# Kernel optimization log

Hardware: AMD Instinct MI355X
Metric: run time of the kernel (lower is better)

The kernel has to match this reference:

```python
import jax, jax.numpy as jnp
import numpy as np

N_NODES = 100_000
EMB = 64
M1 = 500_000   # unary relation ground atoms
M2 = 1_000_000 # binary relation ground atoms


def _mlp_params(key, d_in, d_hid, d_out):
    k1, k2 = jax.random.split(key)
    W1 = jax.random.normal(k1, (d_in, d_hid), jnp.float32) / np.sqrt(d_in)
    W2 = jax.random.normal(k2, (d_hid, d_out), jnp.float32) / np.sqrt(d_hid)
    return W1, jnp.zeros((d_hid,), jnp.float32), W2, jnp.zeros((d_out,), jnp.float32)


def setup_inputs() -> dict:
    key = jax.random.key(0)
    kx, k1, k2, km1, km2, ku = jax.random.split(key, 6)
    node_embeddings = jax.random.normal(kx, (N_NODES, EMB), jnp.float32)
    rel1_idx = jax.random.randint(k1, (M1, 1), 0, N_NODES, jnp.int64)
    rel2_idx = jax.random.randint(k2, (M2, 2), 0, N_NODES, jnp.int64)
    msg1_W1, msg1_b1, msg1_W2, msg1_b2 = _mlp_params(km1, EMB, EMB, EMB)
    msg2_W1, msg2_b1, msg2_W2, msg2_b2 = _mlp_params(km2, 2 * EMB, 2 * EMB, 2 * EMB)
    upd_W1, upd_b1, upd_W2, upd_b2 = _mlp_params(ku, 2 * EMB, EMB, EMB)
    return dict(node_embeddings=node_embeddings, rel1_idx=rel1_idx, rel2_idx=rel2_idx,
                msg1_W1=msg1_W1, msg1_b1=msg1_b1, msg1_W2=msg1_W2, msg1_b2=msg1_b2,
                msg2_W1=msg2_W1, msg2_b1=msg2_b1, msg2_W2=msg2_W2, msg2_b2=msg2_b2,
                upd_W1=upd_W1, upd_b1=upd_b1, upd_W2=upd_W2, upd_b2=upd_b2)


def _relation_messages(node_emb, idx, W1, b1, W2, b2):
    """Gather arity argument embeddings, run MLP, return per-argument messages
    flattened to [M*arity, EMB] plus flat scatter indices [M*arity]."""
    M, arity = idx.shape
    g = node_emb[idx].reshape(M, arity * EMB)          # gather + concat args
    h = jax.nn.relu(g @ W1 + b1)
    m = (h @ W2 + b2).reshape(M * arity, EMB)          # one message per arg slot
    return m, idx.reshape(-1)


def reference(node_embeddings, rel1_idx, rel2_idx,
              msg1_W1, msg1_b1, msg1_W2, msg1_b2,
              msg2_W1, msg2_b1, msg2_W2, msg2_b2,
              upd_W1, upd_b1, upd_W2, upd_b2):
    n = node_embeddings.shape[0]
    # message computation per relation
    m1, i1 = _relation_messages(node_embeddings, rel1_idx, msg1_W1, msg1_b1, msg1_W2, msg1_b2)
    m2, i2 = _relation_messages(node_embeddings, rel2_idx, msg2_W1, msg2_b1, msg2_W2, msg2_b2)
    # scatter-sum aggregation into node slots
    agg = jax.ops.segment_sum(m1, i1, num_segments=n)
    agg = agg + jax.ops.segment_sum(m2, i2, num_segments=n)
    # node update MLP on [node, aggregated]
    u = jnp.concatenate([node_embeddings, agg], axis=-1)   # [N, 2E]
    return jax.nn.relu(u @ upd_W1 + upd_b1) @ upd_W2 + upd_b2
```

## Files before the change

### kernel.cpp

```cpp
#include <hip/hip_runtime.h>
#include <hip/hip_fp16.h>

typedef __bf16 bf16;
typedef bf16 bf16x8 __attribute__((ext_vector_type(8)));
typedef float f32x4 __attribute__((ext_vector_type(4)));

#define LD64  80
#define LD128 144

static __device__ __forceinline__ f32x4 mfma16(bf16x8 a, bf16x8 b, f32x4 c) {
    return __builtin_amdgcn_mfma_f32_16x16x32_bf16(a, b, c, 0, 0, 0);
}

static __device__ __forceinline__ bf16x8 cvt8(float4 a, float4 b) {
    bf16x8 v;
    v[0] = (bf16)a.x; v[1] = (bf16)a.y; v[2] = (bf16)a.z; v[3] = (bf16)a.w;
    v[4] = (bf16)b.x; v[5] = (bf16)b.y; v[6] = (bf16)b.z; v[7] = (bf16)b.w;
    return v;
}

static __device__ __forceinline__ uint32_t pack_bf16(float lo, float hi) {
    bf16 a = (bf16)lo, b = (bf16)hi;
    uint16_t ua = *(uint16_t*)&a, ub = *(uint16_t*)&b;
    return ((uint32_t)ub << 16) | (uint32_t)ua;
}

static __device__ __forceinline__ uint32_t pack_f16(float lo, float hi) {
    __half hl = __float2half_rn(lo), hh = __float2half_rn(hi);
    uint16_t a = *(uint16_t*)&hl, b = *(uint16_t*)&hh;
    return ((uint32_t)b << 16) | (uint32_t)a;
}
static __device__ __forceinline__ void atomic_pk_f16(__half* addr, uint32_t v) {
    asm volatile("global_atomic_pk_add_f16 %0, %1, off" :: "v"(addr), "v"(v) : "memory");
}
static __device__ __forceinline__ float h2f_lo(uint32_t u) {
    uint16_t s = (uint16_t)u; __half h = *(__half*)&s; return __half2float(h);
}
static __device__ __forceinline__ float h2f_hi(uint32_t u) {
    uint16_t s = (uint16_t)(u >> 16); __half h = *(__half*)&s; return __half2float(h);
}

__global__ __launch_bounds__(256) void hist_rk_kernel(
    const int* __restrict__ r1, const int* __restrict__ r2,
    unsigned* __restrict__ cnt1, unsigned* __restrict__ cnt2,
    unsigned short* __restrict__ rk, int M1, int M2x2)
{
    int i = blockIdx.x * 256 + threadIdx.x;
    const int T = gridDim.x * 256;
    const int tot = M1 + M2x2;
    for (; i < tot; i += T) {
        if (i < M1) {
            atomicAdd(&cnt1[r1[i]], 1u);
        } else {
            const int j = i - M1;
            unsigned r = atomicAdd(&cnt2[r2[j]], 1u);
            rk[j] = (unsigned short)r;
        }
    }
}

__global__ __launch_bounds__(256) void scan_sums(
    const unsigned* __restrict__ cnt, unsigned* __restrict__ csum)
{
    __shared__ unsigned s[256];
    const int b = blockIdx.x, t = threadIdx.x;
    s[t] = cnt[b * 512 + t] + cnt[b * 512 + 256 + t];
    __syncthreads();
    for (int d = 128; d > 0; d >>= 1) {
        if (t < d) s[t] += s[t + d];
        __syncthreads();
    }
    if (t == 0) csum[b] = s[0];
}

__global__ __launch_bounds__(256) void scan_chunkoff(unsigned* __restrict__ csum, int nch) {
    __shared__ unsigned s[2][256];
    const int t = threadIdx.x;
    if (nch > 256) {
        if (t == 0) {
            unsigned run = 0;
            for (int j = 0; j < nch; ++j) { unsigned v = csum[j]; csum[j] = run; run += v; }
        }
        return;
    }
    unsigned v = (t < nch) ? csum[t] : 0u;
    s[0][t] = v;
    __syncthreads();
    int src = 0;
    for (int d = 1; d < 256; d <<= 1) {
        int dst = src ^ 1;
        s[dst][t] = s[src][t] + (t >= d ? s[src][t - d] : 0u);
        __syncthreads();
        src = dst;
    }
    if (t < nch) csum[t] = s[src][t] - v;
}

__global__ __launch_bounds__(256) void scan_apply(
    const unsigned* __restrict__ cnt, const unsigned* __restrict__ csum,
    unsigned* __restrict__ rowp)
{
    __shared__ unsigned s[2][512];
    const int b = blockIdx.x, t = threadIdx.x;
    const unsigned base = csum[b];
    s[0][t] = cnt[b * 512 + t];
    s[0][t + 256] = cnt[b * 512 + t + 256];
    __syncthreads();
    int src = 0;
    for (int d = 1; d < 512; d <<= 1) {
        int dst = src ^ 1;
        for (int i = t; i < 512; i += 256)
            s[dst][i] = s[src][i] + (i >= d ? s[src][i - d] : 0u);
        __syncthreads();
        src = dst;
    }
    for (int i = t; i < 512; i += 256)
        rowp[b * 512 + i] = base + s[src][i] - cnt[b * 512 + i];
}

__global__ __launch_bounds__(256) void mix_kernel(
    const int* __restrict__ r2, const unsigned short* __restrict__ rk,
    const unsigned* __restrict__ rowp, int2* __restrict__ sp2,
    int M2x2, int SB,
    const float* __restrict__ emb,
    const float* __restrict__ mW1, const float* __restrict__ mb1,
    const float* __restrict__ r1W1, const float* __restrict__ r1b1,
    const float* __restrict__ r1W2, const float* __restrict__ r1b2,
    bf16* __restrict__ P0, bf16* __restrict__ P1,
    float* __restrict__ aggu, int N, int PT)
{
    __shared__ bf16 sG[64 * LD64];
    __shared__ bf16 sH[64 * LD64];
    __shared__ bf16 sW1t[64 * LD64];
    __shared__ bf16 sW2t[64 * LD64];
    __shared__ float sB1[64], sB2[64];

    const int t = threadIdx.x;

    if ((int)blockIdx.x < SB) {
        const int T = SB * 256;
        for (int i = blockIdx.x * 256 + t; i < M2x2; i += T) {
            const int2 pr = *(const int2*)(r2 + (i & ~1));
            const int slot = i & 1;
            const int n = slot ? pr.y : pr.x;
            const unsigned pos = rowp[n] + (unsigned)rk[i];
            sp2[pos] = make_int2((pr.x << 1) | slot, pr.y);
        }
        return;
    }

    const int bid = blockIdx.x - SB;
    const int G = gridDim.x - SB;
    const int wave = t >> 6, lane = t & 63;
    const int l15 = lane & 15, quad = lane >> 4;
    const int r = t >> 2, p = t & 3;

    for (int i = t; i < 64 * 64; i += 256) {
        int k = i >> 6, n = i & 63;
        sW1t[n * LD64 + k] = (bf16)r1W1[i];
        sW2t[n * LD64 + k] = (bf16)r1W2[i];
    }
    if (t < 64) { sB1[t] = r1b1[t]; sB2[t] = r1b2[t]; }

    bf16x8 wf0[2][2], wf1[2][2];
    float biasv[2];
    #pragma unroll
    for (int j = 0; j < 2; ++j) {
        const int n = (wave * 2 + j) * 16 + l15;
        biasv[j] = mb1[n];
        #pragma unroll
        for (int kt = 0; kt < 2; ++kt) {
            bf16x8 f0, f1;
            #pragma unroll
            for (int e = 0; e < 8; ++e) {
                int k = kt * 32 + quad * 8 + e;
                f0[e] = (bf16)mW1[k * 128 + n];
                f1[e] = (bf16)mW1[(64 + k) * 128 + n];
            }
            wf0[j][kt] = f0;
            wf1[j][kt] = f1;
        }
    }

    for (int tile = bid; tile < PT; tile += G) {
        __syncthreads();
        const int base = tile * 64;
        const int R = base + r;
        if (R < N) {
            const float4* src = (const float4*)(emb + (size_t)R * 64 + p * 16);
            float4 v0 = src[0], v1 = src[1], v2 = src[2], v3 = src[3];
            *(bf16x8*)&sG[r * LD64 + p * 16 + 0] = cvt8(v0, v1);
            *(bf16x8*)&sG[r * LD64 + p * 16 + 8] = cvt8(v2, v3);
        }
        __syncthreads();

        f32x4 a0[4][2], a1[4][2];
        #pragma unroll
        for (int mt = 0; mt < 4; ++mt)
            #pragma unroll
            for (int j = 0; j < 2; ++j) {
                a0[mt][j] = (f32x4){0.f, 0.f, 0.f, 0.f};
                a1[mt][j] = (f32x4){0.f, 0.f, 0.f, 0.f};
            }
        #pragma unroll
        for (int mt = 0; mt < 4; ++mt)
            #pragma unroll
            for (int kt = 0; kt < 2; ++kt) {
                bf16x8 a = *(const bf16x8*)&sG[(mt * 16 + l15) * LD64 + kt * 32 + quad * 8];
                #pragma unroll
                for (int j = 0; j < 2; ++j) {
                    a0[mt][j] = mfma16(a, wf0[j][kt], a0[mt][j]);
                    a1[mt][j] = mfma16(a, wf1[j][kt], a1[mt][j]);
                }
            }
        #pragma unroll
        for (int mt = 0; mt < 4; ++mt)
            #pragma unroll
            for (int j = 0; j < 2; ++j) {
                const int colb = (wave * 2 + j) * 16 + (l15 & ~1);
                const int odd = l15 & 1;
                #pragma unroll
                for (int rr = 0; rr < 4; ++rr) {
                    float v = a0[mt][j][rr] + biasv[j];
                    float o = __shfl_xor(v, 1);
                    float w = a1[mt][j][rr];
                    float ow = __shfl_xor(w, 1);
                    if ((rr >> 1) == odd) {
                        int node = base + mt * 16 + quad * 4 + rr;
                        if (node < N) {
                            *(uint32_t*)&P0[(size_t)node * 128 + colb] =
                                odd ? pack_bf16(o, v) : pack_bf16(v, o);
                            *(uint32_t*)&P1[(size_t)node * 128 + colb] =
                                odd ? pack_bf16(ow, w) : pack_bf16(w, ow);
                        }
                    }
                }
            }

        f32x4 acc[4];
        #pragma unroll
        for (int nt = 0; nt < 4; ++nt) acc[nt] = (f32x4){0.f, 0.f, 0.f, 0.f};
        #pragma unroll
        for (int kt = 0; kt < 2; ++kt) {
            bf16x8 a = *(const bf16x8*)&sG[(wave * 16 + l15) * LD64 + kt * 32 + quad * 8];
            #pragma unroll
            for (int nt = 0; nt < 4; ++nt) {
                bf16x8 bfr = *(const bf16x8*)&sW1t[(nt * 16 + l15) * LD64 + kt * 32 + quad * 8];
                acc[nt] = mfma16(a, bfr, acc[nt]);
            }
        }
        #pragma unroll
        for (int nt = 0; nt < 4; ++nt) {
            float bias = sB1[nt * 16 + l15];
            #pragma unroll
            for (int rr = 0; rr < 4; ++rr) {
                float v = acc[nt][rr] + bias;
                v = v > 0.f ? v : 0.f;
                sH[(wave * 16 + quad * 4 + rr) * LD64 + nt * 16 + l15] = (bf16)v;
            }
        }
        __syncthreads();

        f32x4 acc2[4];
        #pragma unroll
        for (int nt = 0; nt < 4; ++nt) acc2[nt] = (f32x4){0.f, 0.f, 0.f, 0.f};
        #pragma unroll
        for (int kt = 0; kt < 2; ++kt) {
            bf16x8 a = *(const bf16x8*)&sH[(wave * 16 + l15) * LD64 + kt * 32 + quad * 8];
            #pragma unroll
            for (int nt = 0; nt < 4; ++nt) {
                bf16x8 bfr = *(const bf16x8*)&sW2t[(nt * 16 + l15) * LD64 + kt * 32 + quad * 8];
                acc2[nt] = mfma16(a, bfr, acc2[nt]);
            }
        }
        #pragma unroll
        for (int nt = 0; nt < 4; ++nt) {
            float bias = sB2[nt * 16 + l15];
            #pragma unroll
            for (int rr = 0; rr < 4; ++rr) {
                int row = wave * 16 + quad * 4 + rr;
                int R2 = base + row;
                if (R2 < N)
                    aggu[(size_t)R2 * 64 + nt * 16 + l15] = acc2[nt][rr] + bias;
            }
        }
    }
}

__global__ __launch_bounds__(256) void rel2_fused_kernel(
    const bf16* __restrict__ P0, const bf16* __restrict__ P1,
    const int2* __restrict__ sp2,
    const unsigned* __restrict__ rowp, const unsigned* __restrict__ cnt1,
    const float* __restrict__ W2, const float* __restrict__ b2,
    float* agg, int N, int numGroups)
{
    const int HLD = 136;
    __shared__ bf16 hT[2][32 * 136];
    __shared__ float sCf[2][32];

    const int t = threadIdx.x;
    const int wave = t >> 6, lane = t & 63;
    const int l15 = lane & 15, quad = lane >> 4;

    bf16x8 w2f[2][4];
    #pragma unroll
    for (int s = 0; s < 2; ++s)
        #pragma unroll
        for (int kt = 0; kt < 4; ++kt) {
            bf16x8 f;
            #pragma unroll
            for (int e = 0; e < 8; ++e) {
                int k = kt * 32 + quad * 8 + e;
                f[e] = (bf16)W2[k * 128 + s * 64 + wave * 16 + l15];
            }
            w2f[s][kt] = f;
        }
    const int col = wave * 16 + l15;
    const float b2a = b2[col], b2b = b2[64 + col];

    for (int g = blockIdx.x; g < numGroups; g += gridDim.x) {
        const int gb = g * 32;
        __syncthreads();

        for (int k = 0; k < 8; ++k) {
            const int n = gb + wave * 8 + k;
            float a0lo = 0.f, a0hi = 0.f, a1lo = 0.f, a1hi = 0.f;
            float c0 = 0.f, c1 = 0.f;
            if (n < N) {
                unsigned e = rowp[n];
                const unsigned end = rowp[n + 1];
                while (e < end) {
                    const int cnt = (int)min(64u, end - e);
                    int pk = 0, pi1 = 0;
                    if ((int)lane < cnt) {
                        const int2 v = sp2[e + lane];
                        pk = v.x; pi1 = v.y;
                    }
                    unsigned long long bm =
                        __ballot(((int)lane < cnt) && (pk & 1));
                    const int n1 = __popcll(bm);
                    c1 += (float)n1;
                    c0 += (float)(cnt - n1);

                    int j = 0;
                    for (; j + 8 <= cnt; j += 8) {
                        uint32_t d0v[8], d1v[8]; int ajv[8];
                        #pragma unroll
                        for (int q = 0; q < 8; ++q) {
                            const int aj = __shfl(pk, j + q);
                            const int u1 = __shfl(pi1, j + q);
                            ajv[q] = aj;
                            d0v[q] = *(const uint32_t*)(P0 + (size_t)(aj >> 1) * 128 + lane * 2);
                            d1v[q] = *(const uint32_t*)(P1 + (size_t)u1 * 128 + lane * 2);
                        }
                        #pragma unroll
                        for (int q = 0; q < 8; ++q) {
                            float lo = __uint_as_float(d0v[q] << 16) + __uint_as_float(d1v[q] << 16);
                            float hi = __uint_as_float(d0v[q] & 0xffff0000u) + __uint_as_float(d1v[q] & 0xffff0000u);
                            lo = fmaxf(lo, 0.f); hi = fmaxf(hi, 0.f);
                            if (ajv[q] & 1) { a1lo += lo; a1hi += hi; }
                            else            { a0lo += lo; a0hi += hi; }
                        }
                    }
                    for (; j + 4 <= cnt; j += 4) {
                        uint32_t d0v[4], d1v[4]; int ajv[4];
                        #pragma unroll
                        for (int q = 0; q < 4; ++q) {
                            const int aj = __shfl(pk, j + q);
                            const int u1 = __shfl(pi1, j + q);
                            ajv[q] = aj;
                            d0v[q] = *(const uint32_t*)(P0 + (size_t)(aj >> 1) * 128 + lane * 2);
                            d1v[q] = *(const uint32_t*)(P1 + (size_t)u1 * 128 + lane * 2);
                        }
                        #pragma unroll
                        for (int q = 0; q < 4; ++q) {
                            float lo = __uint_as_float(d0v[q] << 16) + __uint_as_float(d1v[q] << 16);
                            float hi = __uint_as_float(d0v[q] & 0xffff0000u) + __uint_as_float(d1v[q] & 0xffff0000u);
                            lo = fmaxf(lo, 0.f); hi = fmaxf(hi, 0.f);
                            if (ajv[q] & 1) { a1lo += lo; a1hi += hi; }
                            else            { a0lo += lo; a0hi += hi; }
                        }
                    }
                    for (; j < cnt; ++j) {
                        const int aj = __shfl(pk, j);
                        const int u1 = __shfl(pi1, j);
                        const uint32_t d0 = *(const uint32_t*)(P0 + (size_t)(aj >> 1) * 128 + lane * 2);
                        const uint32_t d1 = *(const uint32_t*)(P1 + (size_t)u1 * 128 + lane * 2);
                        float lo = __uint_as_float(d0 << 16) + __uint_as_float(d1 << 16);
                        float hi = __uint_as_float(d0 & 0xffff0000u) + __uint_as_float(d1 & 0xffff0000u);
                        lo = fmaxf(lo, 0.f); hi = fmaxf(hi, 0.f);
                        if (aj & 1) { a1lo += lo; a1hi += hi; }
                        else        { a0lo += lo; a0hi += hi; }
                    }
                    e += cnt;
                }
            }
            const int row = wave * 8 + k;
            *(uint32_t*)&hT[0][row * HLD + lane * 2] = pack_bf16(a0lo, a0hi);
            *(uint32_t*)&hT[1][row * HLD + lane * 2] = pack_bf16(a1lo, a1hi);
            if (lane == 0) { sCf[0][row] = c0; sCf[1][row] = c1; }
        }
        __syncthreads();

        f32x4 acc[2];
        #pragma unroll
        for (int mt = 0; mt < 2; ++mt) acc[mt] = (f32x4){0.f, 0.f, 0.f, 0.f};
        #pragma unroll
        for (int s = 0; s < 2; ++s)
            #pragma unroll
            for (int mt = 0; mt < 2; ++mt)
                #pragma unroll
                for (int kt = 0; kt < 4; ++kt) {
                    bf16x8 a = *(const bf16x8*)&hT[s][(mt * 16 + l15) * HLD + kt * 32 + quad * 8];
                    acc[mt] = mfma16(a, w2f[s][kt], acc[mt]);
                }
        #pragma unroll
        for (int mt = 0; mt < 2; ++mt)
            #pragma unroll
            for (int rr = 0; rr < 4; ++rr) {
                const int row = mt * 16 + quad * 4 + rr;
                const int n = gb + row;
                if (n < N) {
                    float* ap = agg + (size_t)n * 64 + col;
                    const float au = *ap;
                    *ap = (float)cnt1[n] * au + acc[mt][rr]
                        + sCf[0][row] * b2a + sCf[1][row] * b2b;
                }
            }
    }
}

__global__ __launch_bounds__(256) void update_kernel(
    const float* __restrict__ emb, const float* agg,
    const float* __restrict__ W1, const float* __restrict__ b1,
    const float* __restrict__ W2, const float* __restrict__ b2,
    float* out, int N, int numTiles)
{
    __shared__ bf16 sW1t[64 * LD128];
    __shared__ bf16 sW2t[64 * LD64];
    __shared__ bf16 sU[64 * LD128];
    __shared__ bf16 sH[64 * LD64];
    __shared__ float sB1[64], sB2[64];

    const int t = threadIdx.x;
    const int wave = t >> 6, lane = t & 63;
    const int l15 = lane & 15, quad = lane >> 4;
    const int r = t >> 2, p = t & 3;

    for (int i = t; i < 128 * 64; i += 256) {
        int k = i >> 6, n = i & 63;
        sW1t[n * LD128 + k] = (bf16)W1[i];
    }
    for (int i = t; i < 64 * 64; i += 256) {
        int k = i >> 6, n = i & 63;
        sW2t[n * LD64 + k] = (bf16)W2[i];
    }
    if (t < 64) { sB1[t] = b1[t]; sB2[t] = b2[t]; }

    for (int tile = blockIdx.x; tile < numTiles; tile += gridDim.x) {
        __syncthreads();
        const int base = tile * 64;
        {
            const int R = base + r;
            if (R < N) {
                const float* srcp = (p < 2) ? (emb + (size_t)R * 64 + p * 32)
                                            : (agg + (size_t)R * 64 + (p - 2) * 32);
                const float4* src = (const float4*)srcp;
                #pragma unroll
                for (int i = 0; i < 4; ++i)
                    *(bf16x8*)&sU[r * LD128 + p * 32 + i * 8] = cvt8(src[2 * i], src[2 * i + 1]);
            }
        }
        __syncthreads();

        f32x4 acc[4];
        #pragma unroll
        for (int nt = 0; nt < 4; ++nt) acc[nt] = (f32x4){0.f, 0.f, 0.f, 0.f};
        #pragma unroll
        for (int kt = 0; kt < 4; ++kt) {
            bf16x8 a = *(const bf16x8*)&sU[(wave * 16 + l15) * LD128 + kt * 32 + quad * 8];
            #pragma unroll
            for (int nt = 0; nt < 4; ++nt) {
                bf16x8 bfr = *(const bf16x8*)&sW1t[(nt * 16 + l15) * LD128 + kt * 32 + quad * 8];
                acc[nt] = mfma16(a, bfr, acc[nt]);
            }
        }
        #pragma unroll
        for (int nt = 0; nt < 4; ++nt) {
            float bias = sB1[nt * 16 + l15];
            #pragma unroll
            for (int rr = 0; rr < 4; ++rr) {
                float v = acc[nt][rr] + bias;
                v = v > 0.f ? v : 0.f;
                sH[(wave * 16 + quad * 4 + rr) * LD64 + nt * 16 + l15] = (bf16)v;
            }
        }
        __syncthreads();

        f32x4 acc2[4];
        #pragma unroll
        for (int nt = 0; nt < 4; ++nt) acc2[nt] = (f32x4){0.f, 0.f, 0.f, 0.f};
        #pragma unroll
        for (int kt = 0; kt < 2; ++kt) {
            bf16x8 a = *(const bf16x8*)&sH[(wave * 16 + l15) * LD64 + kt * 32 + quad * 8];
            #pragma unroll
            for (int nt = 0; nt < 4; ++nt) {
                bf16x8 bfr = *(const bf16x8*)&sW2t[(nt * 16 + l15) * LD64 + kt * 32 + quad * 8];
                acc2[nt] = mfma16(a, bfr, acc2[nt]);
            }
        }
        #pragma unroll
        for (int nt = 0; nt < 4; ++nt) {
            float bias = sB2[nt * 16 + l15];
            #pragma unroll
            for (int rr = 0; rr < 4; ++rr) {
                int row = wave * 16 + quad * 4 + rr;
                int R = base + row;
                if (R < N)
                    out[(size_t)R * 64 + nt * 16 + l15] = acc2[nt][rr] + bias;
            }
        }
    }
}

__global__ __launch_bounds__(256) void rel1_fb_kernel(
    const float* __restrict__ emb, const int* __restrict__ idx,
    const float* __restrict__ W1, const float* __restrict__ b1,
    const float* __restrict__ W2, const float* __restrict__ b2,
    __half* __restrict__ agg, int M, int numTiles)
{
    __shared__ bf16 sW1t[64 * LD64];
    __shared__ bf16 sW2t[64 * LD64];
    __shared__ bf16 sG[64 * LD64];
    __shared__ bf16 sH[64 * LD64];
    __shared__ float sB1[64], sB2[64];
    __shared__ int sIdx[64];

    const int t = threadIdx.x;
    const int wave = t >> 6, lane = t & 63;
    const int l15 = lane & 15, quad = lane >> 4;
    const int r = t >> 2, p = t & 3;

    for (int i = t; i < 64 * 64; i += 256) {
        int k = i >> 6, n = i & 63;
        sW1t[n * LD64 + k] = (bf16)W1[i];
        sW2t[n * LD64 + k] = (bf16)W2[i];
    }
    if (t < 64) { sB1[t] = b1[t]; sB2[t] = b2[t]; }

    for (int tile = blockIdx.x; tile < numTiles; tile += gridDim.x) {
        __syncthreads();
        const int base = tile * 64;
        int id = -1;
        { int R = base + r; if (R < M) id = idx[R]; }
        if (p == 0) sIdx[r] = id;
        if (id >= 0) {
            const float4* src = (const float4*)(emb + (size_t)id * 64 + p * 16);
            float4 v0 = src[0], v1 = src[1], v2 = src[2], v3 = src[3];
            *(bf16x8*)&sG[r * LD64 + p * 16 + 0] = cvt8(v0, v1);
            *(bf16x8*)&sG[r * LD64 + p * 16 + 8] = cvt8(v2, v3);
        }
        __syncthreads();

        f32x4 acc[4];
        #pragma unroll
        for (int nt = 0; nt < 4; ++nt) acc[nt] = (f32x4){0.f, 0.f, 0.f, 0.f};
        #pragma unroll
        for (int kt = 0; kt < 2; ++kt) {
            bf16x8 a = *(const bf16x8*)&sG[(wave * 16 + l15) * LD64 + kt * 32 + quad * 8];
            #pragma unroll
            for (int nt = 0; nt < 4; ++nt) {
                bf16x8 bfr = *(const bf16x8*)&sW1t[(nt * 16 + l15) * LD64 + kt * 32 + quad * 8];
                acc[nt] = mfma16(a, bfr, acc[nt]);
            }
        }
        #pragma unroll
        for (int nt = 0; nt < 4; ++nt) {
            float bias = sB1[nt * 16 + l15];
            #pragma unroll
            for (int rr = 0; rr < 4; ++rr) {
                float v = acc[nt][rr] + bias;
                v = v > 0.f ? v : 0.f;
                sH[(wave * 16 + quad * 4 + rr) * LD64 + nt * 16 + l15] = (bf16)v;
            }
        }
        __syncthreads();

        f32x4 acc2[4];
        #pragma unroll
        for (int nt = 0; nt < 4; ++nt) acc2[nt] = (f32x4){0.f, 0.f, 0.f, 0.f};
        #pragma unroll
        for (int kt = 0; kt < 2; ++kt) {
            bf16x8 a = *(const bf16x8*)&sH[(wave * 16 + l15) * LD64 + kt * 32 + quad * 8];
            #pragma unroll
            for (int nt = 0; nt < 4; ++nt) {
                bf16x8 bfr = *(const bf16x8*)&sW2t[(nt * 16 + l15) * LD64 + kt * 32 + quad * 8];
                acc2[nt] = mfma16(a, bfr, acc2[nt]);
            }
        }
        #pragma unroll
        for (int nt = 0; nt < 4; ++nt) {
            float bias = sB2[nt * 16 + l15];
            const int colb = nt * 16 + (l15 & ~1);
            const int odd = l15 & 1;
            #pragma unroll
            for (int rr = 0; rr < 4; ++rr) {
                float v = acc2[nt][rr] + bias;
                float o = __shfl_xor(v, 1);
                if ((rr >> 1) == odd) {
                    int row = wave * 16 + quad * 4 + rr;
                    int id2 = sIdx[row];
                    if (id2 >= 0)
                        atomic_pk_f16(agg + (size_t)id2 * 64 + colb,
                                      odd ? pack_f16(o, v) : pack_f16(v, o));
                }
            }
        }
    }
}

__global__ __launch_bounds__(256) void rel2_fb_kernel(
    const float* __restrict__ emb, const int* __restrict__ idx,
    const float* __restrict__ W1, const float* __restrict__ b1,
    const float* __restrict__ W2, const float* __restrict__ b2,
    __half* __restrict__ agg, int M, int numTiles)
{
    __shared__ bf16 sG[64 * LD128];
    __shared__ bf16 sH[64 * LD128];
    __shared__ int sIdx[128];

    const int t = threadIdx.x;
    const int wave = t >> 6, lane = t & 63;
    const int l15 = lane & 15, quad = lane >> 4;
    const int r = t >> 2, p = t & 3;

    bf16x8 w1f[2][4], w2f[2][4];
    float bias1[2], bias2[2];
    #pragma unroll
    for (int j = 0; j < 2; ++j) {
        const int n = (wave * 2 + j) * 16 + l15;
        bias1[j] = b1[n];
        bias2[j] = b2[n];
        #pragma unroll
        for (int kt = 0; kt < 4; ++kt) {
            bf16x8 f1, f2;
            #pragma unroll
            for (int e = 0; e < 8; ++e) {
                int k = kt * 32 + quad * 8 + e;
                f1[e] = (bf16)W1[k * 128 + n];
                f2[e] = (bf16)W2[k * 128 + n];
            }
            w1f[j][kt] = f1;
            w2f[j][kt] = f2;
        }
    }

    for (int tile = blockIdx.x; tile < numTiles; tile += gridDim.x) {
        __syncthreads();
        const int base = tile * 64;
        int i0 = -1, i1 = -1;
        { int R = base + r; if (R < M) { i0 = idx[R * 2]; i1 = idx[R * 2 + 1]; } }
        if (p == 0) { sIdx[r * 2] = i0; sIdx[r * 2 + 1] = i1; }
        {
            int myid = (p < 2) ? i0 : i1;
            if (myid >= 0) {
                const float4* src = (const float4*)(emb + (size_t)myid * 64 + (p & 1) * 32);
                #pragma unroll
                for (int i = 0; i < 4; ++i)
                    *(bf16x8*)&sG[r * LD128 + p * 32 + i * 8] = cvt8(src[2 * i], src[2 * i + 1]);
            }
        }
        __syncthreads();

        f32x4 acc[4][2];
        #pragma unroll
        for (int mt = 0; mt < 4; ++mt)
            #pragma unroll
            for (int j = 0; j < 2; ++j) acc[mt][j] = (f32x4){0.f, 0.f, 0.f, 0.f};
        #pragma unroll
        for (int mt = 0; mt < 4; ++mt) {
            #pragma unroll
            for (int kt = 0; kt < 4; ++kt) {
                bf16x8 a = *(const bf16x8*)&sG[(mt * 16 + l15) * LD128 + kt * 32 + quad * 8];
                #pragma unroll
                for (int j = 0; j < 2; ++j) acc[mt][j] = mfma16(a, w1f[j][kt], acc[mt][j]);
            }
        }
        #pragma unroll
        for (int mt = 0; mt < 4; ++mt)
            #pragma unroll
            for (int j = 0; j < 2; ++j) {
                #pragma unroll
                for (int rr = 0; rr < 4; ++rr) {
                    float v = acc[mt][j][rr] + bias1[j];
                    v = v > 0.f ? v : 0.f;
                    sH[(mt * 16 + quad * 4 + rr) * LD128 + (wave * 2 + j) * 16 + l15] = (bf16)v;
                }
            }
        __syncthreads();

        f32x4 acc2[4][2];
        #pragma unroll
        for (int mt = 0; mt < 4; ++mt)
            #pragma unroll
            for (int j = 0; j < 2; ++j) acc2[mt][j] = (f32x4){0.f, 0.f, 0.f, 0.f};
        #pragma unroll
        for (int mt = 0; mt < 4; ++mt) {
            #pragma unroll
            for (int kt = 0; kt < 4; ++kt) {
                bf16x8 a = *(const bf16x8*)&sH[(mt * 16 + l15) * LD128 + kt * 32 + quad * 8];
                #pragma unroll
                for (int j = 0; j < 2; ++j) acc2[mt][j] = mfma16(a, w2f[j][kt], acc2[mt][j]);
            }
        }
        #pragma unroll
        for (int mt = 0; mt < 4; ++mt) {
            #pragma unroll
            for (int j = 0; j < 2; ++j) {
                const int colb = (wave * 2 + j) * 16 + (l15 & ~1);
                const int sel = colb >> 6;
                const int c = colb & 63;
                const int odd = l15 & 1;
                #pragma unroll
                for (int rr = 0; rr < 4; ++rr) {
                    float v = acc2[mt][j][rr] + bias2[j];
                    float o = __shfl_xor(v, 1);
                    if ((rr >> 1) == odd) {
                        int row = mt * 16 + quad * 4 + rr;
                        int id2 = sIdx[row * 2 + sel];
                        if (id2 >= 0)
                            atomic_pk_f16(agg + (size_t)id2 * 64 + c,
                                          odd ? pack_f16(o, v) : pack_f16(v, o));
                    }
                }
            }
        }
    }
}

__global__ __launch_bounds__(256) void update_fb_kernel(
    const float* __restrict__ emb, const __half* __restrict__ agg,
    const float* __restrict__ W1, const float* __restrict__ b1,
    const float* __restrict__ W2, const float* __restrict__ b2,
    float* __restrict__ out, int N, int numTiles)
{
    __shared__ bf16 sW1t[64 * LD128];
    __shared__ bf16 sW2t[64 * LD64];
    __shared__ bf16 sU[64 * LD128];
    __shared__ bf16 sH[64 * LD64];
    __shared__ float sB1[64], sB2[64];

    const int t = threadIdx.x;
    const int wave = t >> 6, lane = t & 63;
    const int l15 = lane & 15, quad = lane >> 4;
    const int r = t >> 2, p = t & 3;

    for (int i = t; i < 128 * 64; i += 256) {
        int k = i >> 6, n = i & 63;
        sW1t[n * LD128 + k] = (bf16)W1[i];
    }
    for (int i = t; i < 64 * 64; i += 256) {
        int k = i >> 6, n = i & 63;
        sW2t[n * LD64 + k] = (bf16)W2[i];
    }
    if (t < 64) { sB1[t] = b1[t]; sB2[t] = b2[t]; }

    for (int tile = blockIdx.x; tile < numTiles; tile += gridDim.x) {
        __syncthreads();
        const int base = tile * 64;
        {
            const int R = base + r;
            if (R < N) {
                if (p < 2) {
                    const float4* src = (const float4*)(emb + (size_t)R * 64 + p * 32);
                    #pragma unroll
                    for (int i = 0; i < 4; ++i)
                        *(bf16x8*)&sU[r * LD128 + p * 32 + i * 8] = cvt8(src[2 * i], src[2 * i + 1]);
                } else {
                    const uint4* src = (const uint4*)(agg + (size_t)R * 64 + (p - 2) * 32);
                    #pragma unroll
                    for (int i = 0; i < 4; ++i) {
                        uint4 u = src[i];
                        bf16x8 o;
                        o[0] = (bf16)h2f_lo(u.x); o[1] = (bf16)h2f_hi(u.x);
                        o[2] = (bf16)h2f_lo(u.y); o[3] = (bf16)h2f_hi(u.y);
                        o[4] = (bf16)h2f_lo(u.z); o[5] = (bf16)h2f_hi(u.z);
                        o[6] = (bf16)h2f_lo(u.w); o[7] = (bf16)h2f_hi(u.w);
                        *(bf16x8*)&sU[r * LD128 + p * 32 + i * 8] = o;
                    }
                }
            }
        }
        __syncthreads();

        f32x4 acc[4];
        #pragma unroll
        for (int nt = 0; nt < 4; ++nt) acc[nt] = (f32x4){0.f, 0.f, 0.f, 0.f};
        #pragma unroll
        for (int kt = 0; kt < 4; ++kt) {
            bf16x8 a = *(const bf16x8*)&sU[(wave * 16 + l15) * LD128 + kt * 32 + quad * 8];
            #pragma unroll
            for (int nt = 0; nt < 4; ++nt) {
                bf16x8 bfr = *(const bf16x8*)&sW1t[(nt * 16 + l15) * LD128 + kt * 32 + quad * 8];
                acc[nt] = mfma16(a, bfr, acc[nt]);
            }
        }
        #pragma unroll
        for (int nt = 0; nt < 4; ++nt) {
            float bias = sB1[nt * 16 + l15];
            #pragma unroll
            for (int rr = 0; rr < 4; ++rr) {
                float v = acc[nt][rr] + bias;
                v = v > 0.f ? v : 0.f;
                sH[(wave * 16 + quad * 4 + rr) * LD64 + nt * 16 + l15] = (bf16)v;
            }
        }
        __syncthreads();

        f32x4 acc2[4];
        #pragma unroll
        for (int nt = 0; nt < 4; ++nt) acc2[nt] = (f32x4){0.f, 0.f, 0.f, 0.f};
        #pragma unroll
        for (int kt = 0; kt < 2; ++kt) {
            bf16x8 a = *(const bf16x8*)&sH[(wave * 16 + l15) * LD64 + kt * 32 + quad * 8];
            #pragma unroll
            for (int nt = 0; nt < 4; ++nt) {
                bf16x8 bfr = *(const bf16x8*)&sW2t[(nt * 16 + l15) * LD64 + kt * 32 + quad * 8];
                acc2[nt] = mfma16(a, bfr, acc2[nt]);
            }
        }
        #pragma unroll
        for (int nt = 0; nt < 4; ++nt) {
            float bias = sB2[nt * 16 + l15];
            #pragma unroll
            for (int rr = 0; rr < 4; ++rr) {
                int row = wave * 16 + quad * 4 + rr;
                int R = base + row;
                if (R < N)
                    out[(size_t)R * 64 + nt * 16 + l15] = acc2[nt][rr] + bias;
            }
        }
    }
}

extern "C" void kernel_launch(void* const* d_in, const int* in_sizes, int n_in,
                              void* d_out, int out_size, void* d_ws, size_t ws_size,
                              hipStream_t stream) {
    const float* emb    = (const float*)d_in[0];
    const int*   rel1   = (const int*)d_in[1];
    const int*   rel2   = (const int*)d_in[2];
    const float* m1W1   = (const float*)d_in[3];
    const float* m1b1   = (const float*)d_in[4];
    const float* m1W2   = (const float*)d_in[5];
    const float* m1b2   = (const float*)d_in[6];
    const float* m2W1   = (const float*)d_in[7];
    const float* m2b1   = (const float*)d_in[8];
    const float* m2W2   = (const float*)d_in[9];
    const float* m2b2   = (const float*)d_in[10];
    const float* uW1    = (const float*)d_in[11];
    const float* ub1    = (const float*)d_in[12];
    const float* uW2    = (const float*)d_in[13];
    const float* ub2    = (const float*)d_in[14];

    const int N    = in_sizes[0] / 64;
    const int M1   = in_sizes[1];
    const int M2x2 = in_sizes[2];
    const int M2   = M2x2 / 2;

    const int nch   = (N + 511) / 512;
    const int nbins = nch * 512;
    const int nbuckets = (N + 31) / 32;
    char* wsb = (char*)d_ws;
    size_t off = 0;
    auto take = [&](size_t bytes) {
        size_t cur = off;
        off = (off + bytes + 255) & ~(size_t)255;
        return cur;
    };
    bf16*           P0   = (bf16*)          (wsb + take((size_t)N * 128 * sizeof(bf16)));
    bf16*           P1   = (bf16*)          (wsb + take((size_t)N * 128 * sizeof(bf16)));
    unsigned*       cnt1 = (unsigned*)      (wsb + take((size_t)nbins * 4));
    unsigned*       cnt2 = (unsigned*)      (wsb + take((size_t)nbins * 4));
    unsigned*       rowp = (unsigned*)      (wsb + take((size_t)nbins * 4));
    unsigned*       csum = (unsigned*)      (wsb + take((size_t)(nch + 64) * 4));
    unsigned short* rk   = (unsigned short*)(wsb + take((size_t)M2x2 * 2));
    int2*           sp2  = (int2*)          (wsb + take((size_t)M2x2 * 8));

    if (off <= ws_size) {
        float* agg = (float*)d_out;

        hipMemsetAsync(cnt1, 0, (size_t)((char*)rowp - (char*)cnt1), stream);

        const int gh = 2048;
        hist_rk_kernel<<<gh, 256, 0, stream>>>(rel1, rel2, cnt1, cnt2, rk, M1, M2x2);

        scan_sums<<<nch, 256, 0, stream>>>(cnt2, csum);
        scan_chunkoff<<<1, 256, 0, stream>>>(csum, nch);
        scan_apply<<<nch, 256, 0, stream>>>(cnt2, csum, rowp);

        const int SB = 2048;
        const int PT = (N + 63) / 64;
        mix_kernel<<<SB + PT, 256, 0, stream>>>(
            rel2, rk, rowp, sp2, M2x2, SB,
            emb, m2W1, m2b1, m1W1, m1b1, m1W2, m1b2,
            P0, P1, agg, N, PT);

        const int gf = nbuckets < 2048 ? nbuckets : 2048;
        rel2_fused_kernel<<<gf, 256, 0, stream>>>(
            P0, P1, sp2, rowp, cnt1, m2W2, m2b2, agg, N, nbuckets);

        update_kernel<<<PT, 256, 0, stream>>>(emb, agg, uW1, ub1, uW2, ub2,
                                              (float*)d_out, N, PT);
    } else {
        __half* aggh = (__half*)d_ws;
        hipMemsetAsync(aggh, 0, (size_t)N * 64 * sizeof(__half), stream);

        const int t1 = (M1 + 63) / 64;
        rel1_fb_kernel<<<t1 < 1024 ? t1 : 1024, 256, 0, stream>>>(
            emb, rel1, m1W1, m1b1, m1W2, m1b2, aggh, M1, t1);
        const int t2 = (M2 + 63) / 64;
        rel2_fb_kernel<<<t2 < 2048 ? t2 : 2048, 256, 0, stream>>>(
            emb, rel2, m2W1, m2b1, m2W2, m2b2, aggh, M2, t2);
        const int tu = (N + 63) / 64;
        update_fb_kernel<<<tu, 256, 0, stream>>>(emb, aggh, uW1, ub1, uW2, ub2,
                                                 (float*)d_out, N, tu);
    }
}
```

Measured before the change: 431.7 us.

## Split per-node edge lists by slot and gather only partner rows

Builds separate histograms for slot-0 and slot-1 occurrences, so each node's CSR segment is partitioned by slot, and stores only the partner index (4 bytes) instead of an int2 per entry. The fused rel2 kernel loads the node's own P0/P1 row once per segment and gathers only the partner's projection per edge. This halves gather traffic per edge and removes the per-edge slot branch and ballot. The cost is an extra counter array and extra reads in the scan kernels.

```diff
diff --git a/kernel.cpp b/kernel.cpp
--- a/kernel.cpp
+++ b/kernel.cpp
@@ -42,29 +42,33 @@
 
 __global__ __launch_bounds__(256) void hist_rk_kernel(
     const int* __restrict__ r1, const int* __restrict__ r2,
-    unsigned* __restrict__ cnt1, unsigned* __restrict__ cnt2,
-    unsigned short* __restrict__ rk, int M1, int M2x2)
+    unsigned* __restrict__ cnt1, unsigned* __restrict__ cntA,
+    unsigned* __restrict__ cntB, ushort2* __restrict__ rk2, int M1, int M2)
 {
     int i = blockIdx.x * 256 + threadIdx.x;
     const int T = gridDim.x * 256;
-    const int tot = M1 + M2x2;
+    const int tot = M1 + M2;
     for (; i < tot; i += T) {
         if (i < M1) {
             atomicAdd(&cnt1[r1[i]], 1u);
         } else {
-            const int j = i - M1;
-            unsigned r = atomicAdd(&cnt2[r2[j]], 1u);
-            rk[j] = (unsigned short)r;
+            const int e = i - M1;
+            const int2 pr = *(const int2*)(r2 + 2 * e);
+            unsigned ra = atomicAdd(&cntA[pr.x], 1u);
+            unsigned rb = atomicAdd(&cntB[pr.y], 1u);
+            rk2[e] = make_ushort2((unsigned short)ra, (unsigned short)rb);
         }
     }
 }
 
 __global__ __launch_bounds__(256) void scan_sums(
-    const unsigned* __restrict__ cnt, unsigned* __restrict__ csum)
+    const unsigned* __restrict__ cntA, const unsigned* __restrict__ cntB,
+    unsigned* __restrict__ csum)
 {
     __shared__ unsigned s[256];
     const int b = blockIdx.x, t = threadIdx.x;
-    s[t] = cnt[b * 512 + t] + cnt[b * 512 + 256 + t];
+    const int x = b * 512 + t, y = x + 256;
+    s[t] = cntA[x] + cntB[x] + cntA[y] + cntB[y];
     __syncthreads();
     for (int d = 128; d > 0; d >>= 1) {
         if (t < d) s[t] += s[t + d];
@@ -97,14 +101,14 @@
 }
 
 __global__ __launch_bounds__(256) void scan_apply(
-    const unsigned* __restrict__ cnt, const unsigned* __restrict__ csum,
-    unsigned* __restrict__ rowp)
+    const unsigned* __restrict__ cntA, const unsigned* __restrict__ cntB,
+    const unsigned* __restrict__ csum, unsigned* __restrict__ rowp)
 {
     __shared__ unsigned s[2][512];
     const int b = blockIdx.x, t = threadIdx.x;
     const unsigned base = csum[b];
-    s[0][t] = cnt[b * 512 + t];
-    s[0][t + 256] = cnt[b * 512 + t + 256];
+    s[0][t] = cntA[b * 512 + t] + cntB[b * 512 + t];
+    s[0][t + 256] = cntA[b * 512 + t + 256] + cntB[b * 512 + t + 256];
     __syncthreads();
     int src = 0;
     for (int d = 1; d < 512; d <<= 1) {
@@ -114,14 +118,16 @@
         __syncthreads();
         src = dst;
     }
-    for (int i = t; i < 512; i += 256)
-        rowp[b * 512 + i] = base + s[src][i] - cnt[b * 512 + i];
+    for (int i = t; i < 512; i += 256) {
+        const unsigned tot = cntA[b * 512 + i] + cntB[b * 512 + i];
+        rowp[b * 512 + i] = base + s[src][i] - tot;
+    }
 }
 
 __global__ __launch_bounds__(256) void mix_kernel(
-    const int* __restrict__ r2, const unsigned short* __restrict__ rk,
-    const unsigned* __restrict__ rowp, int2* __restrict__ sp2,
-    int M2x2, int SB,
+    const int* __restrict__ r2, const ushort2* __restrict__ rk2,
+    const unsigned* __restrict__ rowp, const unsigned* __restrict__ cntA,
+    int* __restrict__ sps, int M2, int SB,
     const float* __restrict__ emb,
     const float* __restrict__ mW1, const float* __restrict__ mb1,
     const float* __restrict__ r1W1, const float* __restrict__ r1b1,
@@ -139,12 +145,11 @@
 
     if ((int)blockIdx.x < SB) {
         const int T = SB * 256;
-        for (int i = blockIdx.x * 256 + t; i < M2x2; i += T) {
-            const int2 pr = *(const int2*)(r2 + (i & ~1));
-            const int slot = i & 1;
-            const int n = slot ? pr.y : pr.x;
-            const unsigned pos = rowp[n] + (unsigned)rk[i];
-            sp2[pos] = make_int2((pr.x << 1) | slot, pr.y);
+        for (int e = blockIdx.x * 256 + t; e < M2; e += T) {
+            const int2 pr = *(const int2*)(r2 + 2 * e);
+            const ushort2 rr = rk2[e];
+            sps[rowp[pr.x] + (unsigned)rr.x] = pr.y;
+            sps[rowp[pr.y] + cntA[pr.y] + (unsigned)rr.y] = pr.x;
         }
         return;
     }
@@ -287,10 +292,63 @@
     }
 }
 
+static __device__ __forceinline__ void seg_walk(
+    const int* __restrict__ sps, unsigned s, const unsigned e,
+    const bf16* __restrict__ P, const int lane,
+    const float clo, const float chi, float& alo, float& ahi)
+{
+    while (s < e) {
+        const int cnt = (int)min(64u, e - s);
+        int pid = 0;
+        if (lane < cnt) pid = sps[s + lane];
+        int j = 0;
+        for (; j + 8 <= cnt; j += 8) {
+            uint32_t dv[8];
+            #pragma unroll
+            for (int q = 0; q < 8; ++q) {
+                const int id = __shfl(pid, j + q);
+                dv[q] = *(const uint32_t*)(P + (size_t)id * 128 + lane * 2);
+            }
+            #pragma unroll
+            for (int q = 0; q < 8; ++q) {
+                float lo = __uint_as_float(dv[q] << 16) + clo;
+                float hi = __uint_as_float(dv[q] & 0xffff0000u) + chi;
+                alo += fmaxf(lo, 0.f);
+                ahi += fmaxf(hi, 0.f);
+            }
+        }
+        for (; j + 4 <= cnt; j += 4) {
+            uint32_t dv[4];
+            #pragma unroll
+            for (int q = 0; q < 4; ++q) {
+                const int id = __shfl(pid, j + q);
+                dv[q] = *(const uint32_t*)(P + (size_t)id * 128 + lane * 2);
+            }
+            #pragma unroll
+            for (int q = 0; q < 4; ++q) {
+                float lo = __uint_as_float(dv[q] << 16) + clo;
+                float hi = __uint_as_float(dv[q] & 0xffff0000u) + chi;
+                alo += fmaxf(lo, 0.f);
+                ahi += fmaxf(hi, 0.f);
+            }
+        }
+        for (; j < cnt; ++j) {
+            const int id = __shfl(pid, j);
+            const uint32_t d = *(const uint32_t*)(P + (size_t)id * 128 + lane * 2);
+            float lo = __uint_as_float(d << 16) + clo;
+            float hi = __uint_as_float(d & 0xffff0000u) + chi;
+            alo += fmaxf(lo, 0.f);
+            ahi += fmaxf(hi, 0.f);
+        }
+        s += cnt;
+    }
+}
+
 __global__ __launch_bounds__(256) void rel2_fused_kernel(
     const bf16* __restrict__ P0, const bf16* __restrict__ P1,
-    const int2* __restrict__ sp2,
-    const unsigned* __restrict__ rowp, const unsigned* __restrict__ cnt1,
+    const int* __restrict__ sps,
+    const unsigned* __restrict__ rowp, const unsigned* __restrict__ cntA,
+    const unsigned* __restrict__ cnt1,
     const float* __restrict__ W2, const float* __restrict__ b2,
     float* agg, int N, int numGroups)
 {
@@ -324,81 +382,30 @@
 
         for (int k = 0; k < 8; ++k) {
             const int n = gb + wave * 8 + k;
-            float a0lo = 0.f, a0hi = 0.f, a1lo = 0.f, a1hi = 0.f;
-            float c0 = 0.f, c1 = 0.f;
+            float h0lo = 0.f, h0hi = 0.f, h1lo = 0.f, h1hi = 0.f;
+            float c0f = 0.f, c1f = 0.f;
             if (n < N) {
-                unsigned e = rowp[n];
-                const unsigned end = rowp[n + 1];
-                while (e < end) {
-                    const int cnt = (int)min(64u, end - e);
-                    int pk = 0, pi1 = 0;
-                    if ((int)lane < cnt) {
-                        const int2 v = sp2[e + lane];
-                        pk = v.x; pi1 = v.y;
-                    }
-                    unsigned long long bm =
-                        __ballot(((int)lane < cnt) && (pk & 1));
-                    const int n1 = __popcll(bm);
-                    c1 += (float)n1;
-                    c0 += (float)(cnt - n1);
-
-                    int j = 0;
-                    for (; j + 8 <= cnt; j += 8) {
-                        uint32_t d0v[8], d1v[8]; int ajv[8];
-                        #pragma unroll
-                        for (int q = 0; q < 8; ++q) {
-                            const int aj = __shfl(pk, j + q);
-                            const int u1 = __shfl(pi1, j + q);
-                            ajv[q] = aj;
-                            d0v[q] = *(const uint32_t*)(P0 + (size_t)(aj >> 1) * 128 + lane * 2);
-                            d1v[q] = *(const uint32_t*)(P1 + (size_t)u1 * 128 + lane * 2);
-                        }
-                        #pragma unroll
-                        for (int q = 0; q < 8; ++q) {
-                            float lo = __uint_as_float(d0v[q] << 16) + __uint_as_float(d1v[q] << 16);
-                            float hi = __uint_as_float(d0v[q] & 0xffff0000u) + __uint_as_float(d1v[q] & 0xffff0000u);
-                            lo = fmaxf(lo, 0.f); hi = fmaxf(hi, 0.f);
-                            if (ajv[q] & 1) { a1lo += lo; a1hi += hi; }
-                            else            { a0lo += lo; a0hi += hi; }
-                        }
-                    }
-                    for (; j + 4 <= cnt; j += 4) {
-                        uint32_t d0v[4], d1v[4]; int ajv[4];
-                        #pragma unroll
-                        for (int q = 0; q < 4; ++q) {
-                            const int aj = __shfl(pk, j + q);
-                            const int u1 = __shfl(pi1, j + q);
-                            ajv[q] = aj;
-                            d0v[q] = *(const uint32_t*)(P0 + (size_t)(aj >> 1) * 128 + lane * 2);
-                            d1v[q] = *(const uint32_t*)(P1 + (size_t)u1 * 128 + lane * 2);
-                        }
-                        #pragma unroll
-                        for (int q = 0; q < 4; ++q) {
-                            float lo = __uint_as_float(d0v[q] << 16) + __uint_as_float(d1v[q] << 16);
-                            float hi = __uint_as_float(d0v[q] & 0xffff0000u) + __uint_as_float(d1v[q] & 0xffff0000u);
-                            lo = fmaxf(lo, 0.f); hi = fmaxf(hi, 0.f);
-                            if (ajv[q] & 1) { a1lo += lo; a1hi += hi; }
-                            else            { a0lo += lo; a0hi += hi; }
-                        }
-                    }
-                    for (; j < cnt; ++j) {
-                        const int aj = __shfl(pk, j);
-                        const int u1 = __shfl(pi1, j);
-                        const uint32_t d0 = *(const uint32_t*)(P0 + (size_t)(aj >> 1) * 128 + lane * 2);
-                        const uint32_t d1 = *(const uint32_t*)(P1 + (size_t)u1 * 128 + lane * 2);
-                        float lo = __uint_as_float(d0 << 16) + __uint_as_float(d1 << 16);
-                        float hi = __uint_as_float(d0 & 0xffff0000u) + __uint_as_float(d1 & 0xffff0000u);
-                        lo = fmaxf(lo, 0.f); hi = fmaxf(hi, 0.f);
-                        if (aj & 1) { a1lo += lo; a1hi += hi; }
-                        else        { a0lo += lo; a0hi += hi; }
-                    }
-                    e += cnt;
+                const unsigned e0 = rowp[n], e1 = rowp[n + 1];
+                const unsigned cA = cntA[n];
+                c0f = (float)cA;
+                c1f = (float)(e1 - e0 - cA);
+                if (cA) {
+                    const uint32_t pd = *(const uint32_t*)(P0 + (size_t)n * 128 + lane * 2);
+                    const float clo = __uint_as_float(pd << 16);
+                    const float chi = __uint_as_float(pd & 0xffff0000u);
+                    seg_walk(sps, e0, e0 + cA, P1, lane, clo, chi, h0lo, h0hi);
                 }
+                if (e1 > e0 + cA) {
+                    const uint32_t pd = *(const uint32_t*)(P1 + (size_t)n * 128 + lane * 2);
+                    const float clo = __uint_as_float(pd << 16);
+                    const float chi = __uint_as_float(pd & 0xffff0000u);
+                    seg_walk(sps, e0 + cA, e1, P0, lane, clo, chi, h1lo, h1hi);
+                }
             }
             const int row = wave * 8 + k;
-            *(uint32_t*)&hT[0][row * HLD + lane * 2] = pack_bf16(a0lo, a0hi);
-            *(uint32_t*)&hT[1][row * HLD + lane * 2] = pack_bf16(a1lo, a1hi);
-            if (lane == 0) { sCf[0][row] = c0; sCf[1][row] = c1; }
+            *(uint32_t*)&hT[0][row * HLD + lane * 2] = pack_bf16(h0lo, h0hi);
+            *(uint32_t*)&hT[1][row * HLD + lane * 2] = pack_bf16(h1lo, h1hi);
+            if (lane == 0) { sCf[0][row] = c0f; sCf[1][row] = c1f; }
         }
         __syncthreads();
 
@@ -877,14 +884,15 @@
         off = (off + bytes + 255) & ~(size_t)255;
         return cur;
     };
-    bf16*           P0   = (bf16*)          (wsb + take((size_t)N * 128 * sizeof(bf16)));
-    bf16*           P1   = (bf16*)          (wsb + take((size_t)N * 128 * sizeof(bf16)));
-    unsigned*       cnt1 = (unsigned*)      (wsb + take((size_t)nbins * 4));
-    unsigned*       cnt2 = (unsigned*)      (wsb + take((size_t)nbins * 4));
-    unsigned*       rowp = (unsigned*)      (wsb + take((size_t)nbins * 4));
-    unsigned*       csum = (unsigned*)      (wsb + take((size_t)(nch + 64) * 4));
-    unsigned short* rk   = (unsigned short*)(wsb + take((size_t)M2x2 * 2));
-    int2*           sp2  = (int2*)          (wsb + take((size_t)M2x2 * 8));
+    bf16*     P0   = (bf16*)    (wsb + take((size_t)N * 128 * sizeof(bf16)));
+    bf16*     P1   = (bf16*)    (wsb + take((size_t)N * 128 * sizeof(bf16)));
+    unsigned* cnt1 = (unsigned*)(wsb + take((size_t)nbins * 4));
+    unsigned* cntA = (unsigned*)(wsb + take((size_t)nbins * 4));
+    unsigned* cntB = (unsigned*)(wsb + take((size_t)nbins * 4));
+    unsigned* rowp = (unsigned*)(wsb + take((size_t)nbins * 4));
+    unsigned* csum = (unsigned*)(wsb + take((size_t)(nch + 64) * 4));
+    ushort2*  rk2  = (ushort2*) (wsb + take((size_t)M2 * 4));
+    int*      sps  = (int*)     (wsb + take((size_t)M2x2 * 4));
 
     if (off <= ws_size) {
         float* agg = (float*)d_out;
@@ -892,22 +900,23 @@
         hipMemsetAsync(cnt1, 0, (size_t)((char*)rowp - (char*)cnt1), stream);
 
         const int gh = 2048;
-        hist_rk_kernel<<<gh, 256, 0, stream>>>(rel1, rel2, cnt1, cnt2, rk, M1, M2x2);
-
-        scan_sums<<<nch, 256, 0, stream>>>(cnt2, csum);
+        hist_rk_kernel<<<gh, 256, 0, stream>>>(rel1, rel2, cnt1, cntA, cntB,
+                                               rk2, M1, M2);
+
+        scan_sums<<<nch, 256, 0, stream>>>(cntA, cntB, csum);
         scan_chunkoff<<<1, 256, 0, stream>>>(csum, nch);
-        scan_apply<<<nch, 256, 0, stream>>>(cnt2, csum, rowp);
+        scan_apply<<<nch, 256, 0, stream>>>(cntA, cntB, csum, rowp);
 
         const int SB = 2048;
         const int PT = (N + 63) / 64;
         mix_kernel<<<SB + PT, 256, 0, stream>>>(
-            rel2, rk, rowp, sp2, M2x2, SB,
+            rel2, rk2, rowp, cntA, sps, M2, SB,
             emb, m2W1, m2b1, m1W1, m1b1, m1W2, m1b2,
             P0, P1, agg, N, PT);
 
         const int gf = nbuckets < 2048 ? nbuckets : 2048;
         rel2_fused_kernel<<<gf, 256, 0, stream>>>(
-            P0, P1, sp2, rowp, cnt1, m2W2, m2b2, agg, N, nbuckets);
+            P0, P1, sps, rowp, cntA, cnt1, m2W2, m2b2, agg, N, nbuckets);
 
         update_kernel<<<PT, 256, 0, stream>>>(emb, agg, uW1, ub1, uW2, ub2,
                                               (float*)d_out, N, PT);
```

Measured after the change: 469.7 us. +8.8%, slower.
